# Kernel optimization log

Measured on AMD Instinct MI355X. Metric: run time of the kernel, lower is better.

The kernel has to match this reference:

```python
import jax, jax.numpy as jnp
import numpy as np

N_EDGES = 2_000_000  # flat batch of edges; last dim = 3 (trans) + 3 (log-scale) + 10 (symmat) + 1 (log-weight)


def _symmatrixvec_to_symmatrix(v):
    # v: [..., 10] upper-triangular coefficients (a..j) of a symmetric 4x4 matrix
    # (matches roma.symmatrixvec_to_symmatrix layout)
    a, b, c, d, e, f, g, h, i, j = [v[..., k] for k in range(10)]
    flat = jnp.stack([a, b, c, d,
                      b, e, f, g,
                      c, f, h, i,
                      d, g, i, j], axis=-1)
    return flat.reshape(v.shape[:-1] + (4, 4))


def setup_inputs() -> dict:
    key = jax.random.key(0)
    edge_preds = jax.random.normal(key, (N_EDGES, 17), dtype=jnp.float32)
    return {"edge_preds": edge_preds}


def reference(edge_preds):
    trans = edge_preds[:, 0:3]
    scale = jnp.exp(edge_preds[:, 3:6])
    # roma.symmatrixvec_to_unitquat: build symmetric 4x4, take eigenvector of
    # the LARGEST eigenvalue (eigh returns ascending order -> last column).
    A = _symmatrixvec_to_symmatrix(edge_preds[:, 6:16].astype(jnp.float32))  # [N,4,4]
    _, eigvecs = jnp.linalg.eigh(A)
    quat = eigvecs[..., :, -1].astype(edge_preds.dtype)  # [N,4] unit quaternion
    weight = jnp.exp(edge_preds[:, 16])
    return (trans, scale, quat, weight)
```

## Files before the change

kernel.cpp:

```cpp
#include <hip/hip_runtime.h>
#include <math.h>

#define TPB 256

typedef float f32x4 __attribute__((ext_vector_type(4)));

#define JROTA(app, aqq, apq, akp, akq, alp, alq)                             \
  do {                                                                       \
    float d_ = 0.5f * ((aqq) - (app));                                       \
    float r_ = __builtin_sqrtf(                                              \
        __builtin_fmaf(d_, d_, __builtin_fmaf((apq), (apq), 1e-30f)));       \
    float u_ = r_ + fabsf(d_);                                               \
    float inv_ = rsqrtf(2.0f * r_ * u_);                                     \
    float c_ = u_ * inv_;                                                    \
    float s_ = (apq)*copysignf(inv_, d_);                                    \
    float sum_ = (app) + (aqq);                                              \
    float c2_ = c_ * c_, s2_ = s_ * s_, cs2_ = 2.0f * c_ * s_;               \
    float napp_ = __builtin_fmaf(c2_, (app),                                 \
                  __builtin_fmaf(s2_, (aqq), -cs2_ * (apq)));                \
    (app) = napp_;                                                           \
    (aqq) = sum_ - napp_;                                                    \
    (apq) = 0.0f;                                                            \
    float nkp_ = c_ * (akp) - s_ * (akq);                                    \
    float nkq_ = s_ * (akp) + c_ * (akq);                                    \
    (akp) = nkp_; (akq) = nkq_;                                              \
    float nlp_ = c_ * (alp) - s_ * (alq);                                    \
    float nlq_ = s_ * (alp) + c_ * (alq);                                    \
    (alp) = nlp_; (alq) = nlq_;                                              \
  } while (0)

__global__ __launch_bounds__(TPB, 4) void pose_post_kernel(
    const float* __restrict__ in, float* __restrict__ out, int n) {
  __shared__ float s_buf[TPB * 17];

  const int tid = threadIdx.x;
  const int wid = tid >> 6;
  const int lane = tid & 63;
  const int we0 = blockIdx.x * TPB + wid * 64;
  const int wavail = min(64, n - we0);
  const bool fullw = (wavail == 64);
  const bool n4 = ((n & 3) == 0);

  float* wbuf = s_buf + wid * (64 * 17);

  if (fullw) {
    const float4* src4 = (const float4*)(in + (size_t)we0 * 17);
    float4* dst4 = (float4*)wbuf;
#pragma unroll
    for (int k = 0; k < 4; ++k) dst4[lane + 64 * k] = src4[lane + 64 * k];
    if (lane < 16) dst4[lane + 256] = src4[lane + 256];
  } else if (wavail > 0) {
    const float* src = in + (size_t)we0 * 17;
    for (int k = lane; k < wavail * 17; k += 64) wbuf[k] = src[k];
  }
  if (lane >= wavail) return;

  float v[17];
#pragma unroll
  for (int j = 0; j < 17; ++j) v[j] = wbuf[lane * 17 + j];

  const int e = we0 + lane;
  const float sc0 = __expf(v[3]), sc1 = __expf(v[4]), sc2 = __expf(v[5]);

  if (fullw && n4) {
    __builtin_amdgcn_wave_barrier();
    wbuf[lane * 3 + 0] = v[0];
    wbuf[lane * 3 + 1] = v[1];
    wbuf[lane * 3 + 2] = v[2];
    wbuf[192 + lane * 3 + 0] = sc0;
    wbuf[192 + lane * 3 + 1] = sc1;
    wbuf[192 + lane * 3 + 2] = sc2;
    __builtin_amdgcn_wave_barrier();
    if (lane < 48) {
      f32x4 t4 = ((const f32x4*)wbuf)[lane];
      f32x4 s4 = ((const f32x4*)(wbuf + 192))[lane];
      __builtin_nontemporal_store(t4, (f32x4*)(out + (size_t)we0 * 3) + lane);
      __builtin_nontemporal_store(
          s4, (f32x4*)(out + (size_t)n * 3 + (size_t)we0 * 3) + lane);
    }
  } else {
    float* otr = out + (size_t)e * 3;
    otr[0] = v[0]; otr[1] = v[1]; otr[2] = v[2];
    float* osc = out + (size_t)n * 3 + (size_t)e * 3;
    osc[0] = sc0; osc[1] = sc1; osc[2] = sc2;
  }
  __builtin_nontemporal_store(__expf(v[16]), out + (size_t)n * 10 + e);

  const float b00 = v[6], b01 = v[7], b02 = v[8], b03 = v[9];
  const float b11 = v[10], b12 = v[11], b13 = v[12];
  const float b22 = v[13], b23 = v[14];
  const float b33 = v[15];

  float a00 = b00, a01 = b01, a02 = b02, a03 = b03;
  float a11 = b11, a12 = b12, a13 = b13;
  float a22 = b22, a23 = b23;
  float a33 = b33;

#pragma unroll
  for (int sweep = 0; sweep < 2; ++sweep) {
    JROTA(a00, a11, a01, a02, a12, a03, a13);
    JROTA(a00, a22, a02, a01, a12, a03, a23);
    JROTA(a00, a33, a03, a01, a13, a02, a23);
    JROTA(a11, a22, a12, a01, a02, a13, a23);
    JROTA(a11, a33, a13, a01, a03, a12, a23);
    JROTA(a22, a33, a23, a02, a03, a12, a13);
  }

  const float lam = fmaxf(fmaxf(a00, a11), fmaxf(a22, a33));

  const float m00 = b00 - lam, m11 = b11 - lam, m22 = b22 - lam,
              m33 = b33 - lam;
  const float m01 = b01, m02 = b02, m03 = b03, m12 = b12, m13 = b13,
              m23 = b23;

  const float p01 = __builtin_fmaf(m02, m13, -m12 * m03);
  const float p02 = __builtin_fmaf(m02, m23, -m22 * m03);
  const float p03 = __builtin_fmaf(m02, m33, -m23 * m03);
  const float p12 = __builtin_fmaf(m12, m23, -m22 * m13);
  const float p13 = __builtin_fmaf(m12, m33, -m23 * m13);
  const float p23 = __builtin_fmaf(m22, m33, -m23 * m23);

  const float c0 = __builtin_fmaf(m11, p23, __builtin_fmaf(-m12, p13, m13 * p12));
  const float c1 = -__builtin_fmaf(m01, p23, __builtin_fmaf(-m12, p03, m13 * p02));
  const float c2 = __builtin_fmaf(m01, p13, __builtin_fmaf(-m11, p03, m13 * p01));
  const float c3 = -__builtin_fmaf(m01, p12, __builtin_fmaf(-m11, p02, m12 * p01));

  const float nrm = rsqrtf(
      __builtin_fmaf(c0, c0,
      __builtin_fmaf(c1, c1,
      __builtin_fmaf(c2, c2, __builtin_fmaf(c3, c3, 1e-30f)))));
  const float q0 = c0 * nrm, q1 = c1 * nrm, q2 = c2 * nrm, q3 = c3 * nrm;

  float* oqbase = out + (size_t)n * 6;
  if ((n & 1) == 0) {
    f32x4 q4 = {q0, q1, q2, q3};
    __builtin_nontemporal_store(q4, (f32x4*)oqbase + e);
  } else {
    oqbase[(size_t)e * 4 + 0] = q0;
    oqbase[(size_t)e * 4 + 1] = q1;
    oqbase[(size_t)e * 4 + 2] = q2;
    oqbase[(size_t)e * 4 + 3] = q3;
  }
}

extern "C" void kernel_launch(void* const* d_in, const int* in_sizes, int n_in,
                              void* d_out, int out_size, void* d_ws,
                              size_t ws_size, hipStream_t stream) {
  const float* in = (const float*)d_in[0];
  float* out = (float*)d_out;
  const int n = in_sizes[0] / 17;
  if (n <= 0) return;
  const int grid = (n + TPB - 1) / TPB;
  pose_post_kernel<<<grid, TPB, 0, stream>>>(in, out, n);
}
```

Before: 44.91 us.

## Load edge records directly from global memory instead of staging through LDS

Drops the cooperative coalesced copy of each wave's 64×17 floats into shared memory. Each thread now reads its own 17-float record with four unaligned 16-byte vector loads plus one scalar load, and LDS shrinks to a small per-wave pack buffer used only for the output transposes. The smaller LDS footprint allows the launch-bounds occupancy hint to rise from 4 to 8. The trade-off is strided, less coalesced global loads, which depend on cache-line reuse across lanes.

```diff
diff --git a/kernel.cpp b/kernel.cpp
--- a/kernel.cpp
+++ b/kernel.cpp
@@ -4,6 +4,7 @@
 #define TPB 256
 
 typedef float f32x4 __attribute__((ext_vector_type(4)));
+typedef float f32x4u __attribute__((ext_vector_type(4), aligned(4)));
 
 #define JROTA(app, aqq, apq, akp, akq, alp, alq)                             \
   do {                                                                       \
@@ -29,51 +30,45 @@
     (alp) = nlp_; (alq) = nlq_;                                              \
   } while (0)
 
-__global__ __launch_bounds__(TPB, 4) void pose_post_kernel(
+__global__ __launch_bounds__(TPB, 8) void pose_post_kernel(
     const float* __restrict__ in, float* __restrict__ out, int n) {
-  __shared__ float s_buf[TPB * 17];
+  __shared__ __align__(16) float s_pack[4][384];
 
   const int tid = threadIdx.x;
   const int wid = tid >> 6;
   const int lane = tid & 63;
+  const int e = blockIdx.x * TPB + tid;
   const int we0 = blockIdx.x * TPB + wid * 64;
-  const int wavail = min(64, n - we0);
-  const bool fullw = (wavail == 64);
+  const bool fullw = (n - we0 >= 64);
   const bool n4 = ((n & 3) == 0);
 
-  float* wbuf = s_buf + wid * (64 * 17);
-
-  if (fullw) {
-    const float4* src4 = (const float4*)(in + (size_t)we0 * 17);
-    float4* dst4 = (float4*)wbuf;
-#pragma unroll
-    for (int k = 0; k < 4; ++k) dst4[lane + 64 * k] = src4[lane + 64 * k];
-    if (lane < 16) dst4[lane + 256] = src4[lane + 256];
-  } else if (wavail > 0) {
-    const float* src = in + (size_t)we0 * 17;
-    for (int k = lane; k < wavail * 17; k += 64) wbuf[k] = src[k];
-  }
-  if (lane >= wavail) return;
+  if (e >= n) return;
 
   float v[17];
-#pragma unroll
-  for (int j = 0; j < 17; ++j) v[j] = wbuf[lane * 17 + j];
+  {
+    const f32x4u* src4 = (const f32x4u*)(in + (size_t)e * 17);
+    f32x4 r0 = src4[0], r1 = src4[1], r2 = src4[2], r3 = src4[3];
+    v[0] = r0.x; v[1] = r0.y; v[2] = r0.z; v[3] = r0.w;
+    v[4] = r1.x; v[5] = r1.y; v[6] = r1.z; v[7] = r1.w;
+    v[8] = r2.x; v[9] = r2.y; v[10] = r2.z; v[11] = r2.w;
+    v[12] = r3.x; v[13] = r3.y; v[14] = r3.z; v[15] = r3.w;
+    v[16] = in[(size_t)e * 17 + 16];
+  }
 
-  const int e = we0 + lane;
   const float sc0 = __expf(v[3]), sc1 = __expf(v[4]), sc2 = __expf(v[5]);
 
   if (fullw && n4) {
-    __builtin_amdgcn_wave_barrier();
-    wbuf[lane * 3 + 0] = v[0];
-    wbuf[lane * 3 + 1] = v[1];
-    wbuf[lane * 3 + 2] = v[2];
-    wbuf[192 + lane * 3 + 0] = sc0;
-    wbuf[192 + lane * 3 + 1] = sc1;
-    wbuf[192 + lane * 3 + 2] = sc2;
+    float* wb = s_pack[wid];
+    wb[lane * 3 + 0] = v[0];
+    wb[lane * 3 + 1] = v[1];
+    wb[lane * 3 + 2] = v[2];
+    wb[192 + lane * 3 + 0] = sc0;
+    wb[192 + lane * 3 + 1] = sc1;
+    wb[192 + lane * 3 + 2] = sc2;
     __builtin_amdgcn_wave_barrier();
     if (lane < 48) {
-      f32x4 t4 = ((const f32x4*)wbuf)[lane];
-      f32x4 s4 = ((const f32x4*)(wbuf + 192))[lane];
+      f32x4 t4 = ((const f32x4*)wb)[lane];
+      f32x4 s4 = ((const f32x4*)(wb + 192))[lane];
       __builtin_nontemporal_store(t4, (f32x4*)(out + (size_t)we0 * 3) + lane);
       __builtin_nontemporal_store(
           s4, (f32x4*)(out + (size_t)n * 3 + (size_t)we0 * 3) + lane);
```

Result: faster. 43.00 us (-4.2%).
